# Optimization experiments

Measured on AMD Instinct MI355X. Metric: run time of the kernel, lower is better.

The kernel has to match this reference:

```python
import jax, jax.numpy as jnp
import numpy as np


def setup_inputs() -> dict:
    key = jax.random.key(0)
    k1, _ = jax.random.split(key)
    x = jax.random.normal(k1, (8, 128, 56, 56), dtype=jnp.float32)
    gamma = jnp.array(0.5, dtype=jnp.float32)  # learned scalar (init gamma=0.5)
    return {"x": x, "gamma": gamma}


def reference(x, gamma):
    # conv=False path: query/key/value convs are Identity, so Q=K=V=x flattened.
    B, C, H, W = x.shape
    N = H * W
    v = x.reshape(B, C, N)                          # [B, C, N]
    # energy[b, i, j] = sum_c x[b, c, i] * x[b, c, j]  (Q^T K)
    energy = jnp.einsum('bci,bcj->bij', v, v)       # [B, N, N]
    # multiplicative mask: zero out the diagonal BEFORE softmax (not -inf)
    mask = 1.0 - jnp.eye(N, dtype=energy.dtype)
    attention = jax.nn.softmax(energy * mask, axis=-1)  # [B, N, N]
    # out = bmm(V, attention): out[b, c, j] = sum_i v[b, c, i] * attention[b, i, j]
    out = jnp.einsum('bci,bij->bcj', v, attention)  # [B, C, N]
    out = jax.nn.relu(out).reshape(B, C, H, W)
    y = gamma * out + x
    return (y, out, x, gamma)
```

## Files before the change

### kernel.cpp

```cpp
#include <hip/hip_runtime.h>
#include <math.h>

#define Bb 8
#define Cc 128
#define Nn 3136
#define Np 3200
#define Mm (Bb*Cc*Nn)
#define PADT 136
#define SHIFT 44.0f

typedef unsigned short u16;
typedef unsigned int   u32;
typedef __attribute__((ext_vector_type(8)))  u16      u16x8;
typedef __attribute__((ext_vector_type(8)))  _Float16 f16x8;
typedef __attribute__((ext_vector_type(4)))  _Float16 f16x4;
typedef __attribute__((ext_vector_type(4)))  float    f32x4;
typedef __attribute__((ext_vector_type(16))) float    f32x16;

__global__ __launch_bounds__(256) void prep_kernel(const float* __restrict__ x,
                                                   const float* __restrict__ gamma_p,
                                                   float* __restrict__ out,
                                                   u16* __restrict__ xt,
                                                   u16* __restrict__ xc,
                                                   float* __restrict__ row_d) {
    const int bx = blockIdx.x;
    const int b = bx / 50, nblk = bx % 50;
    const int t = threadIdx.x;

    if (nblk == 49) {
        const u16x8 z8 = {0, 0, 0, 0, 0, 0, 0, 0};
        #pragma unroll
        for (int it = 0; it < 4; ++it) {
            const int idx = it * 256 + t, row = idx / 17, seg = idx % 17;
            *(u16x8*)&xt[(size_t)(b * Np + Nn + row) * PADT + seg * 8] = z8;
        }
        if (t < 64) {
            const int idx = 1024 + t, row = idx / 17, seg = idx % 17;
            *(u16x8*)&xt[(size_t)(b * Np + Nn + row) * PADT + seg * 8] = z8;
        }
        #pragma unroll
        for (int it = 0; it < 4; ++it) {
            const int idx = it * 256 + t, c = idx >> 3, seg = idx & 7;
            *(u16x8*)&xc[(size_t)(b * Cc + c) * Np + Nn + seg * 8] = z8;
        }
        if (t < 64) row_d[b * Np + Nn + t] = 1.0f;
        return;
    }

    __shared__ float lx[Cc][65];
    const int n0 = nblk * 64;

    #pragma unroll 8
    for (int r = 0; r < 32; ++r) {
        const int c = r * 4 + (t >> 6);
        const int g = (b * Cc + c) * Nn + n0 + (t & 63);
        const float v = x[g];
        lx[c][t & 63] = v;
        out[(size_t)2 * Mm + g] = v;
    }
    __syncthreads();

    {
        const int nl = t & 63, cseg = t >> 6;
        u16x8 hv[4];
        #pragma unroll
        for (int cc = 0; cc < 32; ++cc) {
            const _Float16 hh = (_Float16)lx[cseg * 32 + cc][nl];
            hv[cc >> 3][cc & 7] = __builtin_bit_cast(u16, hh);
        }
        const size_t base = (size_t)(b * Np + n0 + nl) * PADT + cseg * 32;
        #pragma unroll
        for (int k = 0; k < 4; ++k) *(u16x8*)&xt[base + k * 8] = hv[k];
    }
    {
        const int c = t >> 1, half = t & 1;
        u16x8 hv[4];
        #pragma unroll
        for (int k = 0; k < 32; ++k) {
            const _Float16 hh = (_Float16)lx[c][half * 32 + k];
            hv[k >> 3][k & 7] = __builtin_bit_cast(u16, hh);
        }
        const size_t base = (size_t)(b * Cc + c) * Np + n0 + half * 32;
        #pragma unroll
        for (int k = 0; k < 4; ++k) *(u16x8*)&xc[base + k * 8] = hv[k];
    }
    if (bx == 0 && t == 0) out[(size_t)3 * Mm] = gamma_p[0];
}

__global__ __launch_bounds__(256, 3) void stats_kernel(const u16* __restrict__ xt,
                                                       float* __restrict__ row_d) {
    __shared__ u16 s_jt[64 * PADT];

    const int bx = blockIdx.x;
    const int b = bx / 98, rem = bx % 98;
    const int i0 = (rem >> 1) * 64, jh = rem & 1;
    const int t = threadIdx.x;
    const int w = t >> 6, l = t & 63, lane = l & 31, h = l >> 5;
    const int igrp = w & 1, jsub = w >> 1;

    f16x8 Bf[8];
    {
        const size_t rb = (size_t)(b * Np + i0 + igrp * 32 + lane) * PADT + h * 8;
        #pragma unroll
        for (int kk = 0; kk < 8; ++kk)
            Bf[kk] = *(const f16x8*)&xt[rb + kk * 16];
    }

    float sa = 0.0f, sb = 0.0f;
    const int jt0 = jh * 25;

    for (int jt = jt0; jt < jt0 + 25; ++jt) {
        const int j0 = jt * 64;
        __syncthreads();
        {
            u16x8 tv[4], tv4;
            #pragma unroll
            for (int it = 0; it < 4; ++it) {
                const int idx = it * 256 + t, row = idx / 17, seg = idx % 17;
                tv[it] = *(const u16x8*)&xt[(size_t)(b * Np + j0 + row) * PADT + seg * 8];
            }
            if (t < 64) {
                const int idx = 1024 + t, row = idx / 17, seg = idx % 17;
                tv4 = *(const u16x8*)&xt[(size_t)(b * Np + j0 + row) * PADT + seg * 8];
            }
            #pragma unroll
            for (int it = 0; it < 4; ++it) {
                const int idx = it * 256 + t;
                *(u16x8*)&s_jt[(idx / 17) * PADT + (idx % 17) * 8] = tv[it];
            }
            if (t < 64) {
                const int idx = 1024 + t;
                *(u16x8*)&s_jt[(idx / 17) * PADT + (idx % 17) * 8] = tv4;
            }
        }
        __syncthreads();

        f32x16 ea, eb;
        #pragma unroll
        for (int r = 0; r < 16; ++r) { ea[r] = 0.0f; eb[r] = 0.0f; }
        const int arow = (jsub * 32 + lane) * PADT + h * 8;
        #pragma unroll
        for (int kk = 0; kk < 4; ++kk) {
            const f16x8 A0 = *(const f16x8*)&s_jt[arow + (2 * kk) * 16];
            const f16x8 A1 = *(const f16x8*)&s_jt[arow + (2 * kk + 1) * 16];
            ea = __builtin_amdgcn_mfma_f32_32x32x16_f16(A0, Bf[2 * kk], ea, 0, 0, 0);
            eb = __builtin_amdgcn_mfma_f32_32x32x16_f16(A1, Bf[2 * kk + 1], eb, 0, 0, 0);
        }

        const bool diag = (j0 == i0) && (jsub == igrp);
        #pragma unroll
        for (int r = 0; r < 16; ++r) {
            const int mrow = (r & 3) + 8 * (r >> 2) + 4 * h;
            float v = ea[r] + eb[r];
            if (diag && (mrow == lane)) v = 0.0f;
            if (r & 1) sb += __expf(v - SHIFT); else sa += __expf(v - SHIFT);
        }
    }

    float ssum = sa + sb;
    ssum += __shfl_xor(ssum, 32, 64);
    if (h == 0) atomicAdd(&row_d[b * Np + i0 + igrp * 32 + lane], ssum);
}

__global__ __launch_bounds__(512, 2) void out_kernel(const float* __restrict__ x,
                                                     const u16* __restrict__ xt,
                                                     const u16* __restrict__ xc,
                                                     const float* __restrict__ row_d,
                                                     const float* __restrict__ gamma_p,
                                                     float* __restrict__ out) {
    __shared__ u16 s_xt[128 * PADT];
    __shared__ u16 s_xc[128 * PADT];
    __shared__ u16 s_pt[64 * PADT];

    const int bx = blockIdx.x;
    const int b = bx / 49, j0 = (bx % 49) * 64;
    const int t = threadIdx.x;
    const int w = t >> 6, l = t & 63, lane = l & 31, h = l >> 5;
    const int isub = w & 3, jgrp = w >> 2;
    const int ms = w & 3,  jg2 = w >> 2;
    const u16* __restrict__ xtb = xt + (size_t)b * Np * PADT;
    const u16* __restrict__ xcb = xc + (size_t)b * Cc * Np;

    f16x8 Bj[8];
    {
        const size_t rb = (size_t)(j0 + jgrp * 32 + lane) * PADT + h * 8;
        #pragma unroll
        for (int kk = 0; kk < 8; ++kk)
            Bj[kk] = *(const f16x8*)&xtb[rb + kk * 16];
    }

    f32x16 oa, ob;
    #pragma unroll
    for (int r = 0; r < 16; ++r) { oa[r] = 0.0f; ob[r] = 0.0f; }

    for (int ti = 0; ti < 25; ++ti) {
        const int i0g = ti * 128;
        __syncthreads();
        {
            u16x8 vt[4], vt4, vc[4];
            #pragma unroll
            for (int it = 0; it < 4; ++it) {
                const int idx = it * 512 + t, row = idx / 17, seg = idx % 17;
                vt[it] = *(const u16x8*)&xtb[(size_t)(i0g + row) * PADT + seg * 8];
                const int c = idx >> 4, sg = idx & 15;
                vc[it] = *(const u16x8*)&xcb[(size_t)c * Np + i0g + sg * 8];
            }
            if (t < 128) {
                const int idx = 2048 + t, row = idx / 17, seg = idx % 17;
                vt4 = *(const u16x8*)&xtb[(size_t)(i0g + row) * PADT + seg * 8];
            }
            #pragma unroll
            for (int it = 0; it < 4; ++it) {
                const int idx = it * 512 + t;
                *(u16x8*)&s_xt[(idx / 17) * PADT + (idx % 17) * 8] = vt[it];
                *(u16x8*)&s_xc[(idx >> 4) * PADT + (idx & 15) * 8] = vc[it];
            }
            if (t < 128) {
                const int idx = 2048 + t;
                *(u16x8*)&s_xt[(idx / 17) * PADT + (idx % 17) * 8] = vt4;
            }
        }
        __syncthreads();

        f32x4 dq[4];
        #pragma unroll
        for (int q = 0; q < 4; ++q)
            dq[q] = *(const f32x4*)&row_d[b * Np + i0g + isub * 32 + q * 8 + h * 4];

        f32x16 ea, eb;
        #pragma unroll
        for (int r = 0; r < 16; ++r) { ea[r] = 0.0f; eb[r] = 0.0f; }
        const int arow = (isub * 32 + lane) * PADT + h * 8;
        #pragma unroll
        for (int kk = 0; kk < 4; ++kk) {
            const f16x8 A0 = *(const f16x8*)&s_xt[arow + (2 * kk) * 16];
            const f16x8 A1 = *(const f16x8*)&s_xt[arow + (2 * kk + 1) * 16];
            ea = __builtin_amdgcn_mfma_f32_32x32x16_f16(A0, Bj[2 * kk], ea, 0, 0, 0);
            eb = __builtin_amdgcn_mfma_f32_32x32x16_f16(A1, Bj[2 * kk + 1], eb, 0, 0, 0);
        }

        const bool mayDiag = (j0 + 64 > i0g) && (j0 < i0g + 128);
        const int ptbase = (jgrp * 32 + lane) * PADT + isub * 32;
        #pragma unroll
        for (int q = 0; q < 4; ++q) {
            f16x4 pv;
            #pragma unroll
            for (int r = 0; r < 4; ++r) {
                const int m = q * 8 + h * 4 + r;
                float v = ea[q * 4 + r] + eb[q * 4 + r];
                if (mayDiag && (i0g + isub * 32 + m == j0 + jgrp * 32 + lane)) v = 0.0f;
                pv[r] = (_Float16)(__expf(v - SHIFT) * __builtin_amdgcn_rcpf(dq[q][r]));
            }
            *(f16x4*)&s_pt[ptbase + q * 8 + h * 4] = pv;
        }
        __syncthreads();

        const int varow = (ms * 32 + lane) * PADT + h * 8;
        const int pbrow = (jg2 * 32 + lane) * PADT + h * 8;
        #pragma unroll
        for (int kk = 0; kk < 4; ++kk) {
            const f16x8 Av0 = *(const f16x8*)&s_xc[varow + (2 * kk) * 16];
            const f16x8 Bp0 = *(const f16x8*)&s_pt[pbrow + (2 * kk) * 16];
            const f16x8 Av1 = *(const f16x8*)&s_xc[varow + (2 * kk + 1) * 16];
            const f16x8 Bp1 = *(const f16x8*)&s_pt[pbrow + (2 * kk + 1) * 16];
            oa = __builtin_amdgcn_mfma_f32_32x32x16_f16(Av0, Bp0, oa, 0, 0, 0);
            ob = __builtin_amdgcn_mfma_f32_32x32x16_f16(Av1, Bp1, ob, 0, 0, 0);
        }
    }

    const float gamma = gamma_p[0];
    #pragma unroll
    for (int r = 0; r < 16; ++r) {
        const int c = ms * 32 + (r & 3) + 8 * (r >> 2) + 4 * h;
        const size_t pos = (size_t)(b * Cc + c) * Nn + j0 + jg2 * 32 + lane;
        const float o = fmaxf(oa[r] + ob[r], 0.0f);
        out[pos] = fmaf(gamma, o, x[pos]);
        out[(size_t)Mm + pos] = o;
    }
}

extern "C" void kernel_launch(void* const* d_in, const int* in_sizes, int n_in,
                              void* d_out, int out_size, void* d_ws, size_t ws_size,
                              hipStream_t stream) {
    const float* x       = (const float*)d_in[0];
    const float* gamma_p = (const float*)d_in[1];
    float* out = (float*)d_out;

    float* row_d = (float*)d_ws;
    u16* xt = (u16*)((char*)d_ws + (1 << 17));
    u16* xc = xt + (size_t)Bb * Np * PADT;

    hipMemsetAsync(row_d, 0, (size_t)Bb * Np * sizeof(float), stream);
    prep_kernel <<<400, 256, 0, stream>>>(x, gamma_p, out, xt, xc, row_d);
    stats_kernel<<<784, 256, 0, stream>>>(xt, row_d);
    out_kernel  <<<392, 512, 0, stream>>>(x, xt, xc, row_d, gamma_p, out);
}
```

Baseline: 228.4 us.

## Restructure out_kernel to 256 threads with 64-row i-tiles and smaller LDS

The output kernel moves from 512-thread blocks with 128-row i-tiles to 256-thread blocks with 64-row i-tiles and twice as many iterations. LDS buffers shrink, with separate paddings for the xt and xc/P tiles, so three blocks can reside per CU. Each wave now computes 64 channels against one 32-column P block and reuses the P fragment across two MFMAs. Global-to-LDS tile copies become flat contiguous copies, since padded rows are already stored contiguously. The trade-off is twice as many barriers and loop iterations per block, with more occupancy to hide latency in return.

```diff
diff --git a/kernel.cpp b/kernel.cpp
--- a/kernel.cpp
+++ b/kernel.cpp
@@ -6,7 +6,8 @@
 #define Nn 3136
 #define Np 3200
 #define Mm (Bb*Cc*Nn)
-#define PADT 136
+#define PADX 136
+#define PADV 72
 #define SHIFT 44.0f
 
 typedef unsigned short u16;
@@ -32,11 +33,11 @@
         #pragma unroll
         for (int it = 0; it < 4; ++it) {
             const int idx = it * 256 + t, row = idx / 17, seg = idx % 17;
-            *(u16x8*)&xt[(size_t)(b * Np + Nn + row) * PADT + seg * 8] = z8;
+            *(u16x8*)&xt[(size_t)(b * Np + Nn + row) * PADX + seg * 8] = z8;
         }
         if (t < 64) {
             const int idx = 1024 + t, row = idx / 17, seg = idx % 17;
-            *(u16x8*)&xt[(size_t)(b * Np + Nn + row) * PADT + seg * 8] = z8;
+            *(u16x8*)&xt[(size_t)(b * Np + Nn + row) * PADX + seg * 8] = z8;
         }
         #pragma unroll
         for (int it = 0; it < 4; ++it) {
@@ -68,7 +69,7 @@
             const _Float16 hh = (_Float16)lx[cseg * 32 + cc][nl];
             hv[cc >> 3][cc & 7] = __builtin_bit_cast(u16, hh);
         }
-        const size_t base = (size_t)(b * Np + n0 + nl) * PADT + cseg * 32;
+        const size_t base = (size_t)(b * Np + n0 + nl) * PADX + cseg * 32;
         #pragma unroll
         for (int k = 0; k < 4; ++k) *(u16x8*)&xt[base + k * 8] = hv[k];
     }
@@ -89,7 +90,7 @@
 
 __global__ __launch_bounds__(256, 3) void stats_kernel(const u16* __restrict__ xt,
                                                        float* __restrict__ row_d) {
-    __shared__ u16 s_jt[64 * PADT];
+    __shared__ u16 s_jt[64 * PADX];
 
     const int bx = blockIdx.x;
     const int b = bx / 98, rem = bx % 98;
@@ -100,7 +101,7 @@
 
     f16x8 Bf[8];
     {
-        const size_t rb = (size_t)(b * Np + i0 + igrp * 32 + lane) * PADT + h * 8;
+        const size_t rb = (size_t)(b * Np + i0 + igrp * 32 + lane) * PADX + h * 8;
         #pragma unroll
         for (int kk = 0; kk < 8; ++kk)
             Bf[kk] = *(const f16x8*)&xt[rb + kk * 16];
@@ -113,32 +114,23 @@
         const int j0 = jt * 64;
         __syncthreads();
         {
+            const u16* src = xt + (size_t)(b * Np + j0) * PADX;
             u16x8 tv[4], tv4;
             #pragma unroll
-            for (int it = 0; it < 4; ++it) {
-                const int idx = it * 256 + t, row = idx / 17, seg = idx % 17;
-                tv[it] = *(const u16x8*)&xt[(size_t)(b * Np + j0 + row) * PADT + seg * 8];
-            }
-            if (t < 64) {
-                const int idx = 1024 + t, row = idx / 17, seg = idx % 17;
-                tv4 = *(const u16x8*)&xt[(size_t)(b * Np + j0 + row) * PADT + seg * 8];
-            }
-            #pragma unroll
-            for (int it = 0; it < 4; ++it) {
-                const int idx = it * 256 + t;
-                *(u16x8*)&s_jt[(idx / 17) * PADT + (idx % 17) * 8] = tv[it];
-            }
-            if (t < 64) {
-                const int idx = 1024 + t;
-                *(u16x8*)&s_jt[(idx / 17) * PADT + (idx % 17) * 8] = tv4;
-            }
+            for (int it = 0; it < 4; ++it)
+                tv[it] = *(const u16x8*)&src[(it * 256 + t) * 8];
+            if (t < 64) tv4 = *(const u16x8*)&src[(1024 + t) * 8];
+            #pragma unroll
+            for (int it = 0; it < 4; ++it)
+                *(u16x8*)&s_jt[(it * 256 + t) * 8] = tv[it];
+            if (t < 64) *(u16x8*)&s_jt[(1024 + t) * 8] = tv4;
         }
         __syncthreads();
 
         f32x16 ea, eb;
         #pragma unroll
         for (int r = 0; r < 16; ++r) { ea[r] = 0.0f; eb[r] = 0.0f; }
-        const int arow = (jsub * 32 + lane) * PADT + h * 8;
+        const int arow = (jsub * 32 + lane) * PADX + h * 8;
         #pragma unroll
         for (int kk = 0; kk < 4; ++kk) {
             const f16x8 A0 = *(const f16x8*)&s_jt[arow + (2 * kk) * 16];
@@ -162,28 +154,28 @@
     if (h == 0) atomicAdd(&row_d[b * Np + i0 + igrp * 32 + lane], ssum);
 }
 
-__global__ __launch_bounds__(512, 2) void out_kernel(const float* __restrict__ x,
+__global__ __launch_bounds__(256, 3) void out_kernel(const float* __restrict__ x,
                                                      const u16* __restrict__ xt,
                                                      const u16* __restrict__ xc,
                                                      const float* __restrict__ row_d,
                                                      const float* __restrict__ gamma_p,
                                                      float* __restrict__ out) {
-    __shared__ u16 s_xt[128 * PADT];
-    __shared__ u16 s_xc[128 * PADT];
-    __shared__ u16 s_pt[64 * PADT];
+    __shared__ u16 s_xt[64 * PADX];
+    __shared__ u16 s_xc[Cc * PADV];
+    __shared__ u16 s_pt[64 * PADV];
 
     const int bx = blockIdx.x;
     const int b = bx / 49, j0 = (bx % 49) * 64;
     const int t = threadIdx.x;
     const int w = t >> 6, l = t & 63, lane = l & 31, h = l >> 5;
-    const int isub = w & 3, jgrp = w >> 2;
-    const int ms = w & 3,  jg2 = w >> 2;
-    const u16* __restrict__ xtb = xt + (size_t)b * Np * PADT;
+    const int isub = w & 1, jgrp = w >> 1;
+    const int jg = w & 1,  cp = w >> 1;
+    const u16* __restrict__ xtb = xt + (size_t)b * Np * PADX;
     const u16* __restrict__ xcb = xc + (size_t)b * Cc * Np;
 
     f16x8 Bj[8];
     {
-        const size_t rb = (size_t)(j0 + jgrp * 32 + lane) * PADT + h * 8;
+        const size_t rb = (size_t)(j0 + jgrp * 32 + lane) * PADX + h * 8;
         #pragma unroll
         for (int kk = 0; kk < 8; ++kk)
             Bj[kk] = *(const f16x8*)&xtb[rb + kk * 16];
@@ -193,44 +185,33 @@
     #pragma unroll
     for (int r = 0; r < 16; ++r) { oa[r] = 0.0f; ob[r] = 0.0f; }
 
-    for (int ti = 0; ti < 25; ++ti) {
-        const int i0g = ti * 128;
-        __syncthreads();
-        {
-            u16x8 vt[4], vt4, vc[4];
+    for (int ti = 0; ti < 50; ++ti) {
+        const int i0g = ti * 64;
+        __syncthreads();
+        {
+            const u16* srct = xtb + (size_t)i0g * PADX;
+            u16x8 vt[4], vt4, vcr[4];
             #pragma unroll
             for (int it = 0; it < 4; ++it) {
-                const int idx = it * 512 + t, row = idx / 17, seg = idx % 17;
-                vt[it] = *(const u16x8*)&xtb[(size_t)(i0g + row) * PADT + seg * 8];
-                const int c = idx >> 4, sg = idx & 15;
-                vc[it] = *(const u16x8*)&xcb[(size_t)c * Np + i0g + sg * 8];
+                vt[it] = *(const u16x8*)&srct[(it * 256 + t) * 8];
+                const int q = it * 256 + t;
+                vcr[it] = *(const u16x8*)&xcb[(size_t)(q >> 3) * Np + i0g + (q & 7) * 8];
             }
-            if (t < 128) {
-                const int idx = 2048 + t, row = idx / 17, seg = idx % 17;
-                vt4 = *(const u16x8*)&xtb[(size_t)(i0g + row) * PADT + seg * 8];
+            if (t < 64) vt4 = *(const u16x8*)&srct[(1024 + t) * 8];
+            #pragma unroll
+            for (int it = 0; it < 4; ++it) {
+                *(u16x8*)&s_xt[(it * 256 + t) * 8] = vt[it];
+                const int q = it * 256 + t;
+                *(u16x8*)&s_xc[(q >> 3) * PADV + (q & 7) * 8] = vcr[it];
             }
-            #pragma unroll
-            for (int it = 0; it < 4; ++it) {
-                const int idx = it * 512 + t;
-                *(u16x8*)&s_xt[(idx / 17) * PADT + (idx % 17) * 8] = vt[it];
-                *(u16x8*)&s_xc[(idx >> 4) * PADT + (idx & 15) * 8] = vc[it];
-            }
-            if (t < 128) {
-                const int idx = 2048 + t;
-                *(u16x8*)&s_xt[(idx / 17) * PADT + (idx % 17) * 8] = vt4;
-            }
-        }
-        __syncthreads();
-
-        f32x4 dq[4];
-        #pragma unroll
-        for (int q = 0; q < 4; ++q)
-            dq[q] = *(const f32x4*)&row_d[b * Np + i0g + isub * 32 + q * 8 + h * 4];
+            if (t < 64) *(u16x8*)&s_xt[(1024 + t) * 8] = vt4;
+        }
+        __syncthreads();
 
         f32x16 ea, eb;
         #pragma unroll
         for (int r = 0; r < 16; ++r) { ea[r] = 0.0f; eb[r] = 0.0f; }
-        const int arow = (isub * 32 + lane) * PADT + h * 8;
+        const int arow = (isub * 32 + lane) * PADX + h * 8;
         #pragma unroll
         for (int kk = 0; kk < 4; ++kk) {
             const f16x8 A0 = *(const f16x8*)&s_xt[arow + (2 * kk) * 16];
@@ -239,43 +220,55 @@
             eb = __builtin_amdgcn_mfma_f32_32x32x16_f16(A1, Bj[2 * kk + 1], eb, 0, 0, 0);
         }
 
-        const bool mayDiag = (j0 + 64 > i0g) && (j0 < i0g + 128);
-        const int ptbase = (jgrp * 32 + lane) * PADT + isub * 32;
+        const bool mayDiag = (j0 < i0g + 64) && (i0g < j0 + 64);
+        const int ptbase = (jgrp * 32 + lane) * PADV + isub * 32;
         #pragma unroll
         for (int q = 0; q < 4; ++q) {
+            const f32x4 dq = *(const f32x4*)&row_d[b * Np + i0g + isub * 32 + q * 8 + h * 4];
             f16x4 pv;
             #pragma unroll
             for (int r = 0; r < 4; ++r) {
                 const int m = q * 8 + h * 4 + r;
                 float v = ea[q * 4 + r] + eb[q * 4 + r];
                 if (mayDiag && (i0g + isub * 32 + m == j0 + jgrp * 32 + lane)) v = 0.0f;
-                pv[r] = (_Float16)(__expf(v - SHIFT) * __builtin_amdgcn_rcpf(dq[q][r]));
+                pv[r] = (_Float16)(__expf(v - SHIFT) * __builtin_amdgcn_rcpf(dq[r]));
             }
             *(f16x4*)&s_pt[ptbase + q * 8 + h * 4] = pv;
         }
         __syncthreads();
 
-        const int varow = (ms * 32 + lane) * PADT + h * 8;
-        const int pbrow = (jg2 * 32 + lane) * PADT + h * 8;
+        const int pbrow = (jg * 32 + lane) * PADV + h * 8;
+        const int va0 = (cp * 64 + lane) * PADV + h * 8;
+        const int va1 = va0 + 32 * PADV;
         #pragma unroll
         for (int kk = 0; kk < 4; ++kk) {
-            const f16x8 Av0 = *(const f16x8*)&s_xc[varow + (2 * kk) * 16];
-            const f16x8 Bp0 = *(const f16x8*)&s_pt[pbrow + (2 * kk) * 16];
-            const f16x8 Av1 = *(const f16x8*)&s_xc[varow + (2 * kk + 1) * 16];
-            const f16x8 Bp1 = *(const f16x8*)&s_pt[pbrow + (2 * kk + 1) * 16];
-            oa = __builtin_amdgcn_mfma_f32_32x32x16_f16(Av0, Bp0, oa, 0, 0, 0);
-            ob = __builtin_amdgcn_mfma_f32_32x32x16_f16(Av1, Bp1, ob, 0, 0, 0);
+            const f16x8 Bp  = *(const f16x8*)&s_pt[pbrow + kk * 16];
+            const f16x8 Av0 = *(const f16x8*)&s_xc[va0 + kk * 16];
+            const f16x8 Av1 = *(const f16x8*)&s_xc[va1 + kk * 16];
+            oa = __builtin_amdgcn_mfma_f32_32x32x16_f16(Av0, Bp, oa, 0, 0, 0);
+            ob = __builtin_amdgcn_mfma_f32_32x32x16_f16(Av1, Bp, ob, 0, 0, 0);
         }
     }
 
     const float gamma = gamma_p[0];
     #pragma unroll
     for (int r = 0; r < 16; ++r) {
-        const int c = ms * 32 + (r & 3) + 8 * (r >> 2) + 4 * h;
-        const size_t pos = (size_t)(b * Cc + c) * Nn + j0 + jg2 * 32 + lane;
-        const float o = fmaxf(oa[r] + ob[r], 0.0f);
-        out[pos] = fmaf(gamma, o, x[pos]);
-        out[(size_t)Mm + pos] = o;
+        const int mrow = (r & 3) + 8 * (r >> 2) + 4 * h;
+        const int jj = j0 + jg * 32 + lane;
+        {
+            const int c = cp * 64 + mrow;
+            const size_t pos = (size_t)(b * Cc + c) * Nn + jj;
+            const float o = fmaxf(oa[r], 0.0f);
+            out[pos] = fmaf(gamma, o, x[pos]);
+            out[(size_t)Mm + pos] = o;
+        }
+        {
+            const int c = cp * 64 + 32 + mrow;
+            const size_t pos = (size_t)(b * Cc + c) * Nn + jj;
+            const float o = fmaxf(ob[r], 0.0f);
+            out[pos] = fmaf(gamma, o, x[pos]);
+            out[(size_t)Mm + pos] = o;
+        }
     }
 }
 
@@ -288,10 +281,10 @@
 
     float* row_d = (float*)d_ws;
     u16* xt = (u16*)((char*)d_ws + (1 << 17));
-    u16* xc = xt + (size_t)Bb * Np * PADT;
+    u16* xc = xt + (size_t)Bb * Np * PADX;
 
     hipMemsetAsync(row_d, 0, (size_t)Bb * Np * sizeof(float), stream);
     prep_kernel <<<400, 256, 0, stream>>>(x, gamma_p, out, xt, xc, row_d);
     stats_kernel<<<784, 256, 0, stream>>>(xt, row_d);
-    out_kernel  <<<392, 512, 0, stream>>>(x, xt, xc, row_d, gamma_p, out);
-}
+    out_kernel  <<<392, 256, 0, stream>>>(x, xt, xc, row_d, gamma_p, out);
+}
```

Result: faster. 204.8 us (-10.3%).
